# Kernel tuning notes

Hardware: AMD Instinct MI355X
Metric: run time of the kernel (lower is better)

Reference implementation:

```python
import jax, jax.numpy as jnp
import numpy as np

NUM_CLUSTERS = 16
HIDDEN = 1024
BOTTLENECK = 128
N_TOKENS = 65536


def setup_inputs() -> dict:
    key = jax.random.key(0)
    k_h, k_ids, k_w1, k_b1, k_w2, k_b2 = jax.random.split(key, 6)
    h = jax.random.normal(k_h, (N_TOKENS, HIDDEN), dtype=jnp.float32)
    cluster_ids = jax.random.randint(k_ids, (N_TOKENS,), 0, NUM_CLUSTERS)
    # Stacked per-cluster adapter params (torch Linear: y = x @ W.T + b; we store
    # already-transposed weights so forward is x @ W1[c]).
    s1 = 1.0 / np.sqrt(HIDDEN)
    s2 = 1.0 / np.sqrt(BOTTLENECK)
    W1 = jax.random.uniform(k_w1, (NUM_CLUSTERS, HIDDEN, BOTTLENECK), jnp.float32, -s1, s1)
    b1 = jax.random.uniform(k_b1, (NUM_CLUSTERS, BOTTLENECK), jnp.float32, -s1, s1)
    # Original inits these to zero; use small random values so grads are non-trivial.
    W2 = jax.random.uniform(k_w2, (NUM_CLUSTERS, BOTTLENECK, HIDDEN), jnp.float32, -s2, s2) * 0.02
    b2 = jax.random.uniform(k_b2, (NUM_CLUSTERS, HIDDEN), jnp.float32, -s2, s2) * 0.02
    return {"h": h, "cluster_ids": cluster_ids, "W1": W1, "b1": b1, "W2": W2, "b2": b2}


def reference(h, cluster_ids, W1, b1, W2, b2):
    # h: [N, H]; cluster_ids: [N]; W1: [K, H, B]; b1: [K, B]; W2: [K, B, H]; b2: [K, H]
    # out[n] = h[n] + adapter_{cluster_ids[n]}(h[n])
    K = W1.shape[0]
    out = jnp.zeros_like(h)
    for c in range(K):  # fixed small expert count; select per-token result via where
        mid = jax.nn.gelu(h @ W1[c] + b1[c], approximate=False)  # [N, B]
        y = h + mid @ W2[c] + b2[c]                               # [N, H]
        out = jnp.where((cluster_ids == c)[:, None], y, out)
    return out
```

## Files before the change

kernel.cpp:

```cpp
#include <hip/hip_runtime.h>
#include <hip/hip_bf16.h>
#include <math.h>

#define NUM_CLUSTERS 16
#define HIDDEN 1024
#define BOT 128
#define NTOK 65536

typedef __attribute__((ext_vector_type(8))) short bf16x8;
typedef __attribute__((ext_vector_type(4))) float f32x4;

typedef __attribute__((address_space(3))) unsigned int lds_u32;
typedef const __attribute__((address_space(1))) unsigned int glb_u32;

__device__ __forceinline__ void gload16(const void* g, void* l) {
  __builtin_amdgcn_global_load_lds((glb_u32*)g, (lds_u32*)l, 16, 0, 0);
}

__device__ __forceinline__ unsigned short f2bf(float x) {
  union { float f; unsigned u; } v; v.f = x;
  unsigned r = v.u + 0x7fffu + ((v.u >> 16) & 1u);
  return (unsigned short)(r >> 16);
}

__device__ __forceinline__ bf16x8 pack8(float4 a, float4 b) {
  bf16x8 r;
  r[0] = (short)f2bf(a.x); r[1] = (short)f2bf(a.y);
  r[2] = (short)f2bf(a.z); r[3] = (short)f2bf(a.w);
  r[4] = (short)f2bf(b.x); r[5] = (short)f2bf(b.y);
  r[6] = (short)f2bf(b.z); r[7] = (short)f2bf(b.w);
  return r;
}

#define SWZS(row, sidx) ((sidx) ^ (((row) & 7) << 3))
#define SW4(row, fidx) ((fidx) ^ (((row) & 7) << 2))

#define VMW(n) asm volatile("s_waitcnt vmcnt(" #n ")" ::: "memory")
#define SBAR()                                  \
  do {                                          \
    __builtin_amdgcn_sched_barrier(0);          \
    __builtin_amdgcn_s_barrier();               \
    __builtin_amdgcn_sched_barrier(0);          \
  } while (0)
#define LGKM0() asm volatile("s_waitcnt lgkmcnt(0)" ::: "memory")

__device__ __forceinline__ int xcd_swz(int bid, int nwg) {
  const int nx = 8;
  int q = nwg / nx, r = nwg % nx;
  int xcd = bid % nx, idx = bid / nx;
  int b = (xcd < r) ? xcd * (q + 1) : r * (q + 1) + (xcd - r) * q;
  return b + idx;
}


__global__ void k_zero(int* p) {
  if (threadIdx.x < 64) p[threadIdx.x] = 0;
}

__global__ void k_hist(const int* __restrict__ ids, int* __restrict__ counts) {
  __shared__ int lh[NUM_CLUSTERS];
  if (threadIdx.x < NUM_CLUSTERS) lh[threadIdx.x] = 0;
  __syncthreads();
  int i = blockIdx.x * blockDim.x + threadIdx.x;
  int stride = gridDim.x * blockDim.x;
  for (; i < NTOK; i += stride) atomicAdd(&lh[ids[i]], 1);
  __syncthreads();
  if (threadIdx.x < NUM_CLUSTERS) atomicAdd(&counts[threadIdx.x], lh[threadIdx.x]);
}

__global__ void k_scan(const int* __restrict__ counts, int* __restrict__ offsets,
                       int* __restrict__ cursor) {
  if (threadIdx.x == 0 && blockIdx.x == 0) {
    int s = 0;
    for (int c = 0; c < NUM_CLUSTERS; ++c) {
      offsets[c] = s; cursor[c] = s; s += counts[c];
    }
    offsets[NUM_CLUSTERS] = s;
  }
}

__global__ void k_scatter(const int* __restrict__ ids, int* cursor,
                          int* __restrict__ perm) {
  __shared__ int lh[NUM_CLUSTERS], lbase[NUM_CLUSTERS];
  const int tid = threadIdx.x;
  if (tid < NUM_CLUSTERS) lh[tid] = 0;
  __syncthreads();
  const int i = blockIdx.x * 256 + tid;
  const int cc = ids[i];
  const int r = atomicAdd(&lh[cc], 1);
  __syncthreads();
  if (tid < NUM_CLUSTERS) lbase[tid] = atomicAdd(&cursor[tid], lh[tid]);
  __syncthreads();
  perm[lbase[cc] + r] = i;
}

__global__ void k_w1til(const float* __restrict__ W1, unsigned short* __restrict__ outw) {
  const int id = blockIdx.x * 256 + threadIdx.x;
  const int c  = id >> 14;
  const int ks = (id >> 10) & 15;
  const int q  = id & 1023;
  const int o  = q << 4;
  const int row = o >> 7;
  const int lb  = (o & 127) ^ ((row & 7) << 4);
  const int k0  = ks * 64 + (lb >> 1);
  const float* src = W1 + ((size_t)c * HIDDEN + k0) * BOT + row;
  unsigned short v[8];
  #pragma unroll
  for (int j = 0; j < 8; ++j) v[j] = f2bf(src[(size_t)j * BOT]);
  *(uint4*)((char*)outw + ((size_t)(c * 16 + ks)) * 16384 + o) = *(const uint4*)v;
}

__global__ void k_w2til(const float* __restrict__ W2, unsigned short* __restrict__ outw) {
  const int id = blockIdx.x * 256 + threadIdx.x;
  const int c  = id >> 14;
  const int nc = (id >> 10) & 15;
  const int q  = id & 1023;
  const int o  = q << 4;
  const int row = o >> 8;
  const int lb  = (o & 255) ^ ((row & 7) << 4);
  const int b0  = lb >> 1;
  const int n   = nc * 64 + row;
  const float* src = W2 + ((size_t)c * BOT + b0) * HIDDEN + n;
  unsigned short v[8];
  #pragma unroll
  for (int j = 0; j < 8; ++j) v[j] = f2bf(src[(size_t)j * HIDDEN]);
  *(uint4*)((char*)outw + ((size_t)(c * 16 + nc)) * 16384 + o) = *(const uint4*)v;
}

__device__ __forceinline__ bool locate(const int* offsets, int bid, int TMv,
                                       int& c, int& base, int& nvalid) {
  int t = bid;
  for (c = 0; c < NUM_CLUSTERS; ++c) {
    int cnt = offsets[c + 1] - offsets[c];
    int nt = (cnt + TMv - 1) / TMv;
    if (t < nt) {
      base = offsets[c] + t * TMv;
      nvalid = min(TMv, offsets[c + 1] - base);
      return true;
    }
    t -= nt;
  }
  return false;
}


__global__ __launch_bounds__(512, 6) void k_gemm1(
    const float* __restrict__ h, const float* __restrict__ b1g,
    const unsigned short* __restrict__ W1til, const int* __restrict__ offsets,
    const int* __restrict__ perm, unsigned short* __restrict__ midg) {

  __shared__ __align__(16) unsigned short sA[2][4096];
  __shared__ __align__(16) unsigned short sB[2][8192];
  __shared__ int sTok[64];

  const int tid = threadIdx.x;
  const int l = tid & 63, w = tid >> 6;
  const int lr = l & 15, lg = l >> 4;
  const int wr = w >> 2, wc = w & 3;

  const int nwg = NTOK / 64 + NUM_CLUSTERS;
  int c, base, nvalid;
  if (!locate(offsets, xcd_swz(blockIdx.x, nwg), 64, c, base, nvalid)) return;

  if (tid < 64) sTok[tid] = perm[base + min(tid, nvalid - 1)];
  __syncthreads();

  const unsigned short* w1base = W1til + (size_t)c * 16 * 8192;
  const int row = tid >> 3, o8 = tid & 7;
  const float* hrow = h + (long)sTok[row] * HIDDEN + o8 * 8;

  float4 vaA[2], vaB[2];
  vaA[0] = *(const float4*)(hrow);       vaA[1] = *(const float4*)(hrow + 4);
  gload16(w1base + tid * 8, &sB[0][tid * 8]);
  gload16(w1base + 4096 + tid * 8, &sB[0][4096 + tid * 8]);
  vaB[0] = *(const float4*)(hrow + 64);  vaB[1] = *(const float4*)(hrow + 68);
  *(bf16x8*)&sA[0][SWZS(row, row * 64 + o8 * 8)] = pack8(vaA[0], vaA[1]);
  LGKM0();
  SBAR();

  f32x4 acc[2][2];
  #pragma unroll
  for (int i = 0; i < 2; ++i)
    #pragma unroll
    for (int j = 0; j < 2; ++j) { f32x4 z = {0.f, 0.f, 0.f, 0.f}; acc[i][j] = z; }

#define G1_MFMA(CUR)                                                          \
  do {                                                                        \
    _Pragma("unroll")                                                         \
    for (int kk = 0; kk < 2; ++kk) {                                          \
      bf16x8 af[2], bfr[2];                                                   \
      _Pragma("unroll")                                                       \
      for (int mf = 0; mf < 2; ++mf) {                                        \
        const int m = wr * 32 + mf * 16 + lr;                                 \
        af[mf] = *(const bf16x8*)&sA[CUR][SWZS(m, m * 64 + kk * 32 + lg * 8)];\
      }                                                                       \
      _Pragma("unroll")                                                       \
      for (int nf = 0; nf < 2; ++nf) {                                        \
        const int rn = wc * 32 + nf * 16 + lr;                                \
        bfr[nf] = *(const bf16x8*)&sB[CUR][SWZS(rn, rn * 64 + kk * 32 + lg * 8)]; \
      }                                                                       \
      _Pragma("unroll")                                                       \
      for (int mf = 0; mf < 2; ++mf)                                          \
        _Pragma("unroll")                                                     \
        for (int nf = 0; nf < 2; ++nf)                                        \
          acc[mf][nf] = __builtin_amdgcn_mfma_f32_16x16x32_bf16(              \
              af[mf], bfr[nf], acc[mf][nf], 0, 0, 0);                         \
    }                                                                         \
  } while (0)

#define G1_ISSUE_B(T, NXT)                                                    \
  do {                                                                        \
    const unsigned short* w1s = w1base + (T + 1) * 8192;                      \
    gload16(w1s + tid * 8, &sB[NXT][tid * 8]);                                \
    gload16(w1s + 4096 + tid * 8, &sB[NXT][4096 + tid * 8]);                  \
  } while (0)

#define G1_STAGE(SRC, NXT)                                                    \
  do {                                                                        \
    *(bf16x8*)&sA[NXT][SWZS(row, row * 64 + o8 * 8)] = pack8(SRC[0], SRC[1]); \
    LGKM0();                                                                  \
    SBAR();                                                                   \
  } while (0)

  for (int tp = 0; tp < 14; tp += 2) {
    G1_ISSUE_B(tp, 1);
    vaA[0] = *(const float4*)(hrow + (tp + 2) * 64);
    vaA[1] = *(const float4*)(hrow + (tp + 2) * 64 + 4);
    VMW(6);
    SBAR();
    G1_MFMA(0);
    G1_STAGE(vaB, 1);
    G1_ISSUE_B(tp + 1, 0);
    vaB[0] = *(const float4*)(hrow + (tp + 3) * 64);
    vaB[1] = *(const float4*)(hrow + (tp + 3) * 64 + 4);
    VMW(6);
    SBAR();
    G1_MFMA(1);
    G1_STAGE(vaA, 0);
  }
  G1_ISSUE_B(14, 1);
  VMW(4);
  SBAR();
  G1_MFMA(0);
  G1_STAGE(vaB, 1);
  VMW(0);
  SBAR();
  G1_MFMA(1);

  float b1v[2];
  #pragma unroll
  for (int nf = 0; nf < 2; ++nf) b1v[nf] = b1g[c * BOT + wc * 32 + nf * 16 + lr];
  #pragma unroll
  for (int mf = 0; mf < 2; ++mf) {
    #pragma unroll
    for (int nf = 0; nf < 2; ++nf) {
      #pragma unroll
      for (int r = 0; r < 4; ++r) {
        float x = acc[mf][nf][r] + b1v[nf];
        float g = 0.5f * x * (1.0f + erff(x * 0.70710678118654752f));
        const int m = wr * 32 + mf * 16 + lg * 4 + r;
        if (m < nvalid) {
          const int n = wc * 32 + nf * 16 + lr;
          midg[(size_t)(base + m) * BOT + n] = f2bf(g);
        }
      }
    }
  }
}


__global__ __launch_bounds__(512, 6) void k_gemm2(
    const float* __restrict__ h, const float* __restrict__ b2g,
    const unsigned short* __restrict__ W2til, const int* __restrict__ offsets,
    const int* __restrict__ perm, const unsigned short* __restrict__ midg,
    float* __restrict__ out) {

  __shared__ __align__(16) unsigned short sM[8192];
  __shared__ __align__(16) unsigned short sB[2][8192];
  __shared__ int sTok[64];

  const int tid = threadIdx.x;
  const int l = tid & 63, w = tid >> 6;
  const int lr = l & 15, lg = l >> 4;
  const int wr = w >> 2, wc = w & 3;

  const int nwg = NTOK / 64 + NUM_CLUSTERS;
  int c, base, nvalid;
  if (!locate(offsets, xcd_swz(blockIdx.x, nwg), 64, c, base, nvalid)) return;

  if (tid < 64) sTok[tid] = perm[base + min(tid, nvalid - 1)];

  const unsigned short* w2base = W2til + (size_t)c * 16 * 8192;

  {
    const int row = tid >> 3, oct = tid & 7;
    const int srow = base + min(row, nvalid - 1);
    const uint4* ms = (const uint4*)(midg + (size_t)srow * BOT + oct * 16);
    uint4 m0 = ms[0], m1 = ms[1];
    gload16(w2base + tid * 8, &sB[0][tid * 8]);
    gload16(w2base + 4096 + tid * 8, &sB[0][4096 + tid * 8]);
    *(uint4*)&sM[SWZS(row, row * 128 + oct * 16)]     = m0;
    *(uint4*)&sM[SWZS(row, row * 128 + oct * 16 + 8)] = m1;
  }
  LGKM0();
  SBAR();

  const int erow = tid >> 3, eo = tid & 7;
  const long etok = (long)sTok[erow] * HIDDEN;
  const float* hrow = h + etok;
  float* orow = out + etok;
  const bool evalid = erow < nvalid;

  for (int nc = 0; nc < 16; ++nc) {
    const int cur = nc & 1;
    float4 hv0 = *(const float4*)(hrow + nc * 64 + eo * 8);
    float4 hv1 = *(const float4*)(hrow + nc * 64 + eo * 8 + 4);
    float4 bv0 = *(const float4*)(b2g + c * HIDDEN + nc * 64 + eo * 8);
    float4 bv1 = *(const float4*)(b2g + c * HIDDEN + nc * 64 + eo * 8 + 4);
    if (nc < 15) {
      const unsigned short* w2s = w2base + (nc + 1) * 8192;
      gload16(w2s + tid * 8, &sB[cur ^ 1][tid * 8]);
      gload16(w2s + 4096 + tid * 8, &sB[cur ^ 1][4096 + tid * 8]);
    }
    if (nc == 0 || nc == 15) { VMW(6); } else { VMW(8); }
    SBAR();

    f32x4 acc[2];
    { f32x4 z = {0.f, 0.f, 0.f, 0.f}; acc[0] = z; acc[1] = z; }
    #pragma unroll
    for (int kk = 0; kk < 4; ++kk) {
      bf16x8 af[2], bf1;
      #pragma unroll
      for (int mf = 0; mf < 2; ++mf) {
        const int m = wr * 32 + mf * 16 + lr;
        af[mf] = *(const bf16x8*)&sM[SWZS(m, m * 128 + kk * 32 + lg * 8)];
      }
      const int rn = wc * 16 + lr;
      bf1 = *(const bf16x8*)&sB[cur][SWZS(rn, rn * 128 + kk * 32 + lg * 8)];
      #pragma unroll
      for (int mf = 0; mf < 2; ++mf)
        acc[mf] = __builtin_amdgcn_mfma_f32_16x16x32_bf16(af[mf], bf1, acc[mf], 0, 0, 0);
    }
    SBAR();

    float* sOutF = (float*)&sB[cur][0];
    #pragma unroll
    for (int mf = 0; mf < 2; ++mf) {
      #pragma unroll
      for (int r = 0; r < 4; ++r) {
        const int m = wr * 32 + mf * 16 + lg * 4 + r;
        const int n = wc * 16 + lr;
        sOutF[SW4(m, m * 64 + n)] = acc[mf][r];
      }
    }
    LGKM0();
    SBAR();

    if (evalid) {
      const int fb = erow * 64 + eo * 8;
      const float4 y0 = *(const float4*)&sOutF[SW4(erow, fb)];
      const float4 y1 = *(const float4*)&sOutF[SW4(erow, fb + 4)];
      float4 o0, o1;
      o0.x = y0.x + hv0.x + bv0.x; o0.y = y0.y + hv0.y + bv0.y;
      o0.z = y0.z + hv0.z + bv0.z; o0.w = y0.w + hv0.w + bv0.w;
      o1.x = y1.x + hv1.x + bv1.x; o1.y = y1.y + hv1.y + bv1.y;
      o1.z = y1.z + hv1.z + bv1.z; o1.w = y1.w + hv1.w + bv1.w;
      *(float4*)(orow + nc * 64 + eo * 8)     = o0;
      *(float4*)(orow + nc * 64 + eo * 8 + 4) = o1;
    }
    SBAR();
  }
}

#define FSWZ(row, sidx) ((sidx) ^ (((row) & 7) << 3))

__global__ __launch_bounds__(256, 2) void k_fused(
    const float* __restrict__ h, const float* __restrict__ b1g,
    const float* __restrict__ b2g, const unsigned short* __restrict__ W1til,
    const unsigned short* __restrict__ W2til, const int* __restrict__ offsets,
    const int* __restrict__ perm, float* __restrict__ out) {

  __shared__ __align__(16) unsigned short sAB[16384];
  __shared__ __align__(16) unsigned short sMid[16384];
  __shared__ int sTok[128];

  const int tid = threadIdx.x;
  const int l = tid & 63, w = tid >> 6;
  const int wr = w >> 1, wc = w & 1;
  const int lr = l & 15, lg = l >> 4;

  int c, base, nvalid;
  if (!locate(offsets, blockIdx.x, 128, c, base, nvalid)) return;

  if (tid < 128) sTok[tid] = perm[base + min(tid, nvalid - 1)];
  __syncthreads();

  const unsigned short* w1base = W1til + (size_t)c * 16 * 8192;
  const unsigned short* w2base = W2til + (size_t)c * 16 * 8192;

  const int arow = tid >> 1, ahalf = tid & 1;
  const long htok = (long)sTok[arow] * HIDDEN;

  f32x4 acc[4][4];
  #pragma unroll
  for (int i = 0; i < 4; ++i)
    #pragma unroll
    for (int j = 0; j < 4; ++j) { f32x4 z = {0.f, 0.f, 0.f, 0.f}; acc[i][j] = z; }

  for (int ks = 0; ks < 16; ++ks) {
    __syncthreads();
    const unsigned short* w1s = w1base + ks * 8192;
    #pragma unroll
    for (int j = 0; j < 4; ++j)
      gload16(w1s + j * 2048 + tid * 8, &sAB[8192 + j * 2048 + tid * 8]);
    {
      const float* hp = h + htok + ks * 64 + ahalf * 32;
      float4 v0 = *(const float4*)(hp + 0),  v1 = *(const float4*)(hp + 4);
      float4 v2 = *(const float4*)(hp + 8),  v3 = *(const float4*)(hp + 12);
      float4 v4 = *(const float4*)(hp + 16), v5 = *(const float4*)(hp + 20);
      float4 v6 = *(const float4*)(hp + 24), v7 = *(const float4*)(hp + 28);
      const int sb = arow * 64 + ahalf * 32;
      *(bf16x8*)&sAB[FSWZ(arow, sb + 0)]  = pack8(v0, v1);
      *(bf16x8*)&sAB[FSWZ(arow, sb + 8)]  = pack8(v2, v3);
      *(bf16x8*)&sAB[FSWZ(arow, sb + 16)] = pack8(v4, v5);
      *(bf16x8*)&sAB[FSWZ(arow, sb + 24)] = pack8(v6, v7);
    }
    __syncthreads();
    #pragma unroll
    for (int kk = 0; kk < 2; ++kk) {
      bf16x8 af[4], bfr[4];
      #pragma unroll
      for (int mf = 0; mf < 4; ++mf) {
        const int row = wr * 64 + mf * 16 + lr;
        af[mf] = *(const bf16x8*)&sAB[FSWZ(row, row * 64 + kk * 32 + lg * 8)];
      }
      #pragma unroll
      for (int nf = 0; nf < 4; ++nf) {
        const int rn = wc * 64 + nf * 16 + lr;
        bfr[nf] = *(const bf16x8*)&sAB[8192 + FSWZ(rn, rn * 64 + kk * 32 + lg * 8)];
      }
      #pragma unroll
      for (int mf = 0; mf < 4; ++mf)
        #pragma unroll
        for (int nf = 0; nf < 4; ++nf)
          acc[mf][nf] = __builtin_amdgcn_mfma_f32_16x16x32_bf16(af[mf], bfr[nf], acc[mf][nf], 0, 0, 0);
    }
  }

  float b1v[4];
  #pragma unroll
  for (int nf = 0; nf < 4; ++nf) b1v[nf] = b1g[c * BOT + wc * 64 + nf * 16 + lr];
  #pragma unroll
  for (int mf = 0; mf < 4; ++mf)
    #pragma unroll
    for (int nf = 0; nf < 4; ++nf)
      #pragma unroll
      for (int r = 0; r < 4; ++r) {
        float x = acc[mf][nf][r] + b1v[nf];
        float g = 0.5f * x * (1.0f + erff(x * 0.70710678118654752f));
        const int m = wr * 64 + mf * 16 + lg * 4 + r;
        const int n = wc * 64 + nf * 16 + lr;
        sMid[FSWZ(m, m * 128 + n)] = f2bf(g);
      }

  for (int nc = 0; nc < 16; ++nc) {
    __syncthreads();
    #pragma unroll
    for (int j = 0; j < 4; ++j)
      gload16(w2base + nc * 8192 + j * 2048 + tid * 8, &sAB[j * 2048 + tid * 8]);
    __syncthreads();

    f32x4 a2[4][2];
    #pragma unroll
    for (int i = 0; i < 4; ++i)
      #pragma unroll
      for (int j = 0; j < 2; ++j) { f32x4 z = {0.f, 0.f, 0.f, 0.f}; a2[i][j] = z; }

    #pragma unroll
    for (int kk = 0; kk < 4; ++kk) {
      bf16x8 af[4], bfr[2];
      #pragma unroll
      for (int mf = 0; mf < 4; ++mf) {
        const int m = wr * 64 + mf * 16 + lr;
        af[mf] = *(const bf16x8*)&sMid[FSWZ(m, m * 128 + kk * 32 + lg * 8)];
      }
      #pragma unroll
      for (int nf = 0; nf < 2; ++nf) {
        const int rn = wc * 32 + nf * 16 + lr;
        bfr[nf] = *(const bf16x8*)&sAB[FSWZ(rn, rn * 128 + kk * 32 + lg * 8)];
      }
      #pragma unroll
      for (int mf = 0; mf < 4; ++mf)
        #pragma unroll
        for (int nf = 0; nf < 2; ++nf)
          a2[mf][nf] = __builtin_amdgcn_mfma_f32_16x16x32_bf16(af[mf], bfr[nf], a2[mf][nf], 0, 0, 0);
    }

    #pragma unroll
    for (int nf = 0; nf < 2; ++nf) {
      const int nn = nc * 64 + wc * 32 + nf * 16 + lr;
      const float b2v = b2g[c * HIDDEN + nn];
      #pragma unroll
      for (int mf = 0; mf < 4; ++mf)
        #pragma unroll
        for (int r = 0; r < 4; ++r) {
          const int m = wr * 64 + mf * 16 + lg * 4 + r;
          if (m < nvalid) {
            const long tk = (long)sTok[m] * HIDDEN;
            out[tk + nn] = h[tk + nn] + a2[mf][nf][r] + b2v;
          }
        }
    }
  }
}

extern "C" void kernel_launch(void* const* d_in, const int* in_sizes, int n_in,
                              void* d_out, int out_size, void* d_ws, size_t ws_size,
                              hipStream_t stream) {
  const float* h   = (const float*)d_in[0];
  const int*   ids = (const int*)d_in[1];
  const float* W1  = (const float*)d_in[2];
  const float* b1  = (const float*)d_in[3];
  const float* W2  = (const float*)d_in[4];
  const float* b2  = (const float*)d_in[5];
  float* out = (float*)d_out;

  char* ws = (char*)d_ws;
  int* counts  = (int*)ws;
  int* cursor  = (int*)(ws + 64);
  int* offsets = (int*)(ws + 128);
  int* perm    = (int*)(ws + 256);
  unsigned short* W1til = (unsigned short*)(ws + 262400);
  unsigned short* W2til = W1til + (size_t)16 * 16 * 8192;
  unsigned short* midg  = W2til + (size_t)16 * 16 * 8192;
  const size_t need = 262400 + 2 * (size_t)16 * 16 * 8192 * 2 +
                      (size_t)NTOK * BOT * 2;

  k_zero<<<1, 64, 0, stream>>>(counts);
  k_hist<<<256, 256, 0, stream>>>(ids, counts);
  k_scan<<<1, 64, 0, stream>>>(counts, offsets, cursor);
  k_scatter<<<NTOK / 256, 256, 0, stream>>>(ids, cursor, perm);
  k_w1til<<<1024, 256, 0, stream>>>(W1, W1til);
  k_w2til<<<1024, 256, 0, stream>>>(W2, W2til);

  if (ws_size >= need) {
    const int nwg = NTOK / 64 + NUM_CLUSTERS;
    k_gemm1<<<nwg, 512, 0, stream>>>(h, b1, W1til, offsets, perm, midg);
    k_gemm2<<<nwg, 512, 0, stream>>>(h, b2, W2til, offsets, perm, midg, out);
  } else {
    k_fused<<<NTOK / 128 + NUM_CLUSTERS, 256, 0, stream>>>(
        h, b1, b2, W1til, W2til, offsets, perm, out);
  }
}
```

Measured before the change: 269.9 us.

## Process two token tiles per workgroup in gemm kernels and tighten wait scheduling

Both grouped GEMM kernels now launch half as many workgroups, and each one loops over two consecutive 64-token tiles. The per-tile prologue is repeated inside the loop. The vmcnt waits are wrapped in sched_barriers and the loads are pinned in place, with waits changed to depend on the pipeline stage. The aim is to cut workgroup launch and tail overhead and to get more predictable overlap of loads with MFMA. The cost is less parallelism, and the second tile's prologue is serialized after the first tile's epilogue.

```diff
diff --git a/kernel.cpp b/kernel.cpp
--- a/kernel.cpp
+++ b/kernel.cpp
@@ -6,6 +6,7 @@
 #define HIDDEN 1024
 #define BOT 128
 #define NTOK 65536
+#define NPAIRS ((NTOK / 64 + NUM_CLUSTERS) / 2)
 
 typedef __attribute__((ext_vector_type(8))) short bf16x8;
 typedef __attribute__((ext_vector_type(4))) float f32x4;
@@ -35,12 +36,18 @@
 #define SWZS(row, sidx) ((sidx) ^ (((row) & 7) << 3))
 #define SW4(row, fidx) ((fidx) ^ (((row) & 7) << 2))
 
-#define VMW(n) asm volatile("s_waitcnt vmcnt(" #n ")" ::: "memory")
+#define SCB() __builtin_amdgcn_sched_barrier(0)
+#define VMW(n)                                          \
+  do {                                                  \
+    SCB();                                              \
+    asm volatile("s_waitcnt vmcnt(" #n ")" ::: "memory"); \
+    SCB();                                              \
+  } while (0)
 #define SBAR()                                  \
   do {                                          \
-    __builtin_amdgcn_sched_barrier(0);          \
+    SCB();                                      \
     __builtin_amdgcn_s_barrier();               \
-    __builtin_amdgcn_sched_barrier(0);          \
+    SCB();                                      \
   } while (0)
 #define LGKM0() asm volatile("s_waitcnt lgkmcnt(0)" ::: "memory")
 
@@ -157,32 +164,9 @@
   const int l = tid & 63, w = tid >> 6;
   const int lr = l & 15, lg = l >> 4;
   const int wr = w >> 2, wc = w & 3;
-
-  const int nwg = NTOK / 64 + NUM_CLUSTERS;
-  int c, base, nvalid;
-  if (!locate(offsets, xcd_swz(blockIdx.x, nwg), 64, c, base, nvalid)) return;
-
-  if (tid < 64) sTok[tid] = perm[base + min(tid, nvalid - 1)];
-  __syncthreads();
-
-  const unsigned short* w1base = W1til + (size_t)c * 16 * 8192;
   const int row = tid >> 3, o8 = tid & 7;
-  const float* hrow = h + (long)sTok[row] * HIDDEN + o8 * 8;
-
-  float4 vaA[2], vaB[2];
-  vaA[0] = *(const float4*)(hrow);       vaA[1] = *(const float4*)(hrow + 4);
-  gload16(w1base + tid * 8, &sB[0][tid * 8]);
-  gload16(w1base + 4096 + tid * 8, &sB[0][4096 + tid * 8]);
-  vaB[0] = *(const float4*)(hrow + 64);  vaB[1] = *(const float4*)(hrow + 68);
-  *(bf16x8*)&sA[0][SWZS(row, row * 64 + o8 * 8)] = pack8(vaA[0], vaA[1]);
-  LGKM0();
-  SBAR();
-
-  f32x4 acc[2][2];
-  #pragma unroll
-  for (int i = 0; i < 2; ++i)
-    #pragma unroll
-    for (int j = 0; j < 2; ++j) { f32x4 z = {0.f, 0.f, 0.f, 0.f}; acc[i][j] = z; }
+
+  const int pair = xcd_swz(blockIdx.x, NPAIRS);
 
 #define G1_MFMA(CUR)                                                          \
   do {                                                                        \
@@ -208,64 +192,87 @@
     }                                                                         \
   } while (0)
 
-#define G1_ISSUE_B(T, NXT)                                                    \
-  do {                                                                        \
-    const unsigned short* w1s = w1base + (T + 1) * 8192;                      \
-    gload16(w1s + tid * 8, &sB[NXT][tid * 8]);                                \
-    gload16(w1s + 4096 + tid * 8, &sB[NXT][4096 + tid * 8]);                  \
-  } while (0)
-
-#define G1_STAGE(SRC, NXT)                                                    \
-  do {                                                                        \
-    *(bf16x8*)&sA[NXT][SWZS(row, row * 64 + o8 * 8)] = pack8(SRC[0], SRC[1]); \
-    LGKM0();                                                                  \
-    SBAR();                                                                   \
-  } while (0)
-
-  for (int tp = 0; tp < 14; tp += 2) {
-    G1_ISSUE_B(tp, 1);
-    vaA[0] = *(const float4*)(hrow + (tp + 2) * 64);
-    vaA[1] = *(const float4*)(hrow + (tp + 2) * 64 + 4);
-    VMW(6);
+  for (int tt = 0; tt < 2; ++tt) {
+    int c, base, nvalid;
+    if (!locate(offsets, pair * 2 + tt, 64, c, base, nvalid)) break;
+
+    if (tid < 64) sTok[tid] = perm[base + min(tid, nvalid - 1)];
+    LGKM0();
     SBAR();
-    G1_MFMA(0);
-    G1_STAGE(vaB, 1);
-    G1_ISSUE_B(tp + 1, 0);
-    vaB[0] = *(const float4*)(hrow + (tp + 3) * 64);
-    vaB[1] = *(const float4*)(hrow + (tp + 3) * 64 + 4);
-    VMW(6);
+
+    const unsigned short* w1base = W1til + (size_t)c * 16 * 8192;
+    const float* hrow = h + (long)sTok[row] * HIDDEN + o8 * 8;
+
+    float4 vaA[2], vaB[2];
+    vaA[0] = *(const float4*)(hrow);       vaA[1] = *(const float4*)(hrow + 4);
+    SCB();
+    gload16(w1base + tid * 8, &sB[0][tid * 8]);
+    gload16(w1base + 4096 + tid * 8, &sB[0][4096 + tid * 8]);
+    SCB();
+    vaB[0] = *(const float4*)(hrow + 64);  vaB[1] = *(const float4*)(hrow + 68);
+    SCB();
+    *(bf16x8*)&sA[0][SWZS(row, row * 64 + o8 * 8)] = pack8(vaA[0], vaA[1]);
+    LGKM0();
+    VMW(2);
     SBAR();
-    G1_MFMA(1);
-    G1_STAGE(vaA, 0);
-  }
-  G1_ISSUE_B(14, 1);
-  VMW(4);
-  SBAR();
-  G1_MFMA(0);
-  G1_STAGE(vaB, 1);
-  VMW(0);
-  SBAR();
-  G1_MFMA(1);
-
-  float b1v[2];
-  #pragma unroll
-  for (int nf = 0; nf < 2; ++nf) b1v[nf] = b1g[c * BOT + wc * 32 + nf * 16 + lr];
-  #pragma unroll
-  for (int mf = 0; mf < 2; ++mf) {
-    #pragma unroll
-    for (int nf = 0; nf < 2; ++nf) {
-      #pragma unroll
-      for (int r = 0; r < 4; ++r) {
-        float x = acc[mf][nf][r] + b1v[nf];
-        float g = 0.5f * x * (1.0f + erff(x * 0.70710678118654752f));
-        const int m = wr * 32 + mf * 16 + lg * 4 + r;
-        if (m < nvalid) {
-          const int n = wc * 32 + nf * 16 + lr;
-          midg[(size_t)(base + m) * BOT + n] = f2bf(g);
+
+    f32x4 acc[2][2];
+    #pragma unroll
+    for (int i = 0; i < 2; ++i)
+      #pragma unroll
+      for (int j = 0; j < 2; ++j) { f32x4 z = {0.f, 0.f, 0.f, 0.f}; acc[i][j] = z; }
+
+    #pragma unroll
+    for (int t = 0; t < 16; ++t) {
+      const int cur = t & 1;
+      if (t < 15) {
+        const unsigned short* w1s = w1base + (t + 1) * 8192;
+        gload16(w1s + tid * 8, &sB[cur ^ 1][tid * 8]);
+        gload16(w1s + 4096 + tid * 8, &sB[cur ^ 1][4096 + tid * 8]);
+        SCB();
+      }
+      if (t < 14) {
+        if (t & 1) {
+          vaB[0] = *(const float4*)(hrow + (t + 2) * 64);
+          vaB[1] = *(const float4*)(hrow + (t + 2) * 64 + 4);
+        } else {
+          vaA[0] = *(const float4*)(hrow + (t + 2) * 64);
+          vaA[1] = *(const float4*)(hrow + (t + 2) * 64 + 4);
         }
-      }
-    }
-  }
+        SCB();
+      }
+      G1_MFMA(cur);
+      if (t < 15) {
+        const float4* src = ((t + 1) & 1) ? vaB : vaA;
+        *(bf16x8*)&sA[cur ^ 1][SWZS(row, row * 64 + o8 * 8)] = pack8(src[0], src[1]);
+        if (t < 14) { VMW(2); } else { VMW(0); }
+        LGKM0();
+        SBAR();
+      }
+    }
+
+    float b1v[2];
+    #pragma unroll
+    for (int nf = 0; nf < 2; ++nf) b1v[nf] = b1g[c * BOT + wc * 32 + nf * 16 + lr];
+    #pragma unroll
+    for (int mf = 0; mf < 2; ++mf) {
+      #pragma unroll
+      for (int nf = 0; nf < 2; ++nf) {
+        #pragma unroll
+        for (int r = 0; r < 4; ++r) {
+          float x = acc[mf][nf][r] + b1v[nf];
+          float g = 0.5f * x * (1.0f + erff(x * 0.70710678118654752f));
+          const int m = wr * 32 + mf * 16 + lg * 4 + r;
+          if (m < nvalid) {
+            const int n = wc * 32 + nf * 16 + lr;
+            midg[(size_t)(base + m) * BOT + n] = f2bf(g);
+          }
+        }
+      }
+    }
+    VMW(0);
+  }
+#undef G1_MFMA
 }
 
 
@@ -283,92 +290,100 @@
   const int l = tid & 63, w = tid >> 6;
   const int lr = l & 15, lg = l >> 4;
   const int wr = w >> 2, wc = w & 3;
-
-  const int nwg = NTOK / 64 + NUM_CLUSTERS;
-  int c, base, nvalid;
-  if (!locate(offsets, xcd_swz(blockIdx.x, nwg), 64, c, base, nvalid)) return;
-
-  if (tid < 64) sTok[tid] = perm[base + min(tid, nvalid - 1)];
-
-  const unsigned short* w2base = W2til + (size_t)c * 16 * 8192;
-
-  {
-    const int row = tid >> 3, oct = tid & 7;
-    const int srow = base + min(row, nvalid - 1);
-    const uint4* ms = (const uint4*)(midg + (size_t)srow * BOT + oct * 16);
-    uint4 m0 = ms[0], m1 = ms[1];
-    gload16(w2base + tid * 8, &sB[0][tid * 8]);
-    gload16(w2base + 4096 + tid * 8, &sB[0][4096 + tid * 8]);
-    *(uint4*)&sM[SWZS(row, row * 128 + oct * 16)]     = m0;
-    *(uint4*)&sM[SWZS(row, row * 128 + oct * 16 + 8)] = m1;
-  }
-  LGKM0();
-  SBAR();
-
   const int erow = tid >> 3, eo = tid & 7;
-  const long etok = (long)sTok[erow] * HIDDEN;
-  const float* hrow = h + etok;
-  float* orow = out + etok;
-  const bool evalid = erow < nvalid;
-
-  for (int nc = 0; nc < 16; ++nc) {
-    const int cur = nc & 1;
-    float4 hv0 = *(const float4*)(hrow + nc * 64 + eo * 8);
-    float4 hv1 = *(const float4*)(hrow + nc * 64 + eo * 8 + 4);
-    float4 bv0 = *(const float4*)(b2g + c * HIDDEN + nc * 64 + eo * 8);
-    float4 bv1 = *(const float4*)(b2g + c * HIDDEN + nc * 64 + eo * 8 + 4);
-    if (nc < 15) {
-      const unsigned short* w2s = w2base + (nc + 1) * 8192;
-      gload16(w2s + tid * 8, &sB[cur ^ 1][tid * 8]);
-      gload16(w2s + 4096 + tid * 8, &sB[cur ^ 1][4096 + tid * 8]);
-    }
-    if (nc == 0 || nc == 15) { VMW(6); } else { VMW(8); }
+
+  const int pair = xcd_swz(blockIdx.x, NPAIRS);
+
+  for (int tt = 0; tt < 2; ++tt) {
+    int c, base, nvalid;
+    if (!locate(offsets, pair * 2 + tt, 64, c, base, nvalid)) break;
+
+    if (tid < 64) sTok[tid] = perm[base + min(tid, nvalid - 1)];
+
+    const unsigned short* w2base = W2til + (size_t)c * 16 * 8192;
+
+    {
+      const int srow = base + min(erow, nvalid - 1);
+      const uint4* ms = (const uint4*)(midg + (size_t)srow * BOT + eo * 16);
+      uint4 m0 = ms[0], m1 = ms[1];
+      SCB();
+      gload16(w2base + tid * 8, &sB[0][tid * 8]);
+      gload16(w2base + 4096 + tid * 8, &sB[0][4096 + tid * 8]);
+      SCB();
+      *(uint4*)&sM[SWZS(erow, erow * 128 + eo * 16)]     = m0;
+      *(uint4*)&sM[SWZS(erow, erow * 128 + eo * 16 + 8)] = m1;
+    }
+    LGKM0();
+    VMW(0);
     SBAR();
 
-    f32x4 acc[2];
-    { f32x4 z = {0.f, 0.f, 0.f, 0.f}; acc[0] = z; acc[1] = z; }
-    #pragma unroll
-    for (int kk = 0; kk < 4; ++kk) {
-      bf16x8 af[2], bf1;
+    const long etok = (long)sTok[erow] * HIDDEN;
+    const float* hrow = h + etok;
+    float* orow = out + etok;
+    const bool evalid = erow < nvalid;
+
+    for (int nc = 0; nc < 16; ++nc) {
+      const int cur = nc & 1;
+      float4 hv0 = *(const float4*)(hrow + nc * 64 + eo * 8);
+      float4 hv1 = *(const float4*)(hrow + nc * 64 + eo * 8 + 4);
+      float4 bv0 = *(const float4*)(b2g + c * HIDDEN + nc * 64 + eo * 8);
+      float4 bv1 = *(const float4*)(b2g + c * HIDDEN + nc * 64 + eo * 8 + 4);
+      SCB();
+      if (nc < 15) {
+        const unsigned short* w2s = w2base + (nc + 1) * 8192;
+        gload16(w2s + tid * 8, &sB[cur ^ 1][tid * 8]);
+        gload16(w2s + 4096 + tid * 8, &sB[cur ^ 1][4096 + tid * 8]);
+        SCB();
+      }
+
+      f32x4 acc[2];
+      { f32x4 z = {0.f, 0.f, 0.f, 0.f}; acc[0] = z; acc[1] = z; }
+      #pragma unroll
+      for (int kk = 0; kk < 4; ++kk) {
+        bf16x8 af[2], bf1;
+        #pragma unroll
+        for (int mf = 0; mf < 2; ++mf) {
+          const int m = wr * 32 + mf * 16 + lr;
+          af[mf] = *(const bf16x8*)&sM[SWZS(m, m * 128 + kk * 32 + lg * 8)];
+        }
+        const int rn = wc * 16 + lr;
+        bf1 = *(const bf16x8*)&sB[cur][SWZS(rn, rn * 128 + kk * 32 + lg * 8)];
+        #pragma unroll
+        for (int mf = 0; mf < 2; ++mf)
+          acc[mf] = __builtin_amdgcn_mfma_f32_16x16x32_bf16(af[mf], bf1, acc[mf], 0, 0, 0);
+      }
+      SBAR();
+
+      float* sOutF = (float*)&sB[cur][0];
       #pragma unroll
       for (int mf = 0; mf < 2; ++mf) {
-        const int m = wr * 32 + mf * 16 + lr;
-        af[mf] = *(const bf16x8*)&sM[SWZS(m, m * 128 + kk * 32 + lg * 8)];
-      }
-      const int rn = wc * 16 + lr;
-      bf1 = *(const bf16x8*)&sB[cur][SWZS(rn, rn * 128 + kk * 32 + lg * 8)];
-      #pragma unroll
-      for (int mf = 0; mf < 2; ++mf)
-        acc[mf] = __builtin_amdgcn_mfma_f32_16x16x32_bf16(af[mf], bf1, acc[mf], 0, 0, 0);
-    }
-    SBAR();
-
-    float* sOutF = (float*)&sB[cur][0];
-    #pragma unroll
-    for (int mf = 0; mf < 2; ++mf) {
-      #pragma unroll
-      for (int r = 0; r < 4; ++r) {
-        const int m = wr * 32 + mf * 16 + lg * 4 + r;
-        const int n = wc * 16 + lr;
-        sOutF[SW4(m, m * 64 + n)] = acc[mf][r];
-      }
-    }
-    LGKM0();
-    SBAR();
-
-    if (evalid) {
-      const int fb = erow * 64 + eo * 8;
-      const float4 y0 = *(const float4*)&sOutF[SW4(erow, fb)];
-      const float4 y1 = *(const float4*)&sOutF[SW4(erow, fb + 4)];
-      float4 o0, o1;
-      o0.x = y0.x + hv0.x + bv0.x; o0.y = y0.y + hv0.y + bv0.y;
-      o0.z = y0.z + hv0.z + bv0.z; o0.w = y0.w + hv0.w + bv0.w;
-      o1.x = y1.x + hv1.x + bv1.x; o1.y = y1.y + hv1.y + bv1.y;
-      o1.z = y1.z + hv1.z + bv1.z; o1.w = y1.w + hv1.w + bv1.w;
-      *(float4*)(orow + nc * 64 + eo * 8)     = o0;
-      *(float4*)(orow + nc * 64 + eo * 8 + 4) = o1;
-    }
-    SBAR();
+        #pragma unroll
+        for (int r = 0; r < 4; ++r) {
+          const int m = wr * 32 + mf * 16 + lg * 4 + r;
+          const int n = wc * 16 + lr;
+          sOutF[SW4(m, m * 64 + n)] = acc[mf][r];
+        }
+      }
+      LGKM0();
+      SBAR();
+
+      if (evalid) {
+        const int fb = erow * 64 + eo * 8;
+        const float4 y0 = *(const float4*)&sOutF[SW4(erow, fb)];
+        const float4 y1 = *(const float4*)&sOutF[SW4(erow, fb + 4)];
+        float4 o0, o1;
+        o0.x = y0.x + hv0.x + bv0.x; o0.y = y0.y + hv0.y + bv0.y;
+        o0.z = y0.z + hv0.z + bv0.z; o0.w = y0.w + hv0.w + bv0.w;
+        o1.x = y1.x + hv1.x + bv1.x; o1.y = y1.y + hv1.y + bv1.y;
+        o1.z = y1.z + hv1.z + bv1.z; o1.w = y1.w + hv1.w + bv1.w;
+        *(float4*)(orow + nc * 64 + eo * 8)     = o0;
+        *(float4*)(orow + nc * 64 + eo * 8 + 4) = o1;
+      }
+      if (nc < 15) {
+        VMW(2);
+        SBAR();
+      }
+    }
   }
 }
 
@@ -431,8 +446,8 @@
       bf16x8 af[4], bfr[4];
       #pragma unroll
       for (int mf = 0; mf < 4; ++mf) {
-        const int row = wr * 64 + mf * 16 + lr;
-        af[mf] = *(const bf16x8*)&sAB[FSWZ(row, row * 64 + kk * 32 + lg * 8)];
+        const int rw = wr * 64 + mf * 16 + lr;
+        af[mf] = *(const bf16x8*)&sAB[FSWZ(rw, rw * 64 + kk * 32 + lg * 8)];
       }
       #pragma unroll
       for (int nf = 0; nf < 4; ++nf) {
@@ -544,9 +559,8 @@
   k_w2til<<<1024, 256, 0, stream>>>(W2, W2til);
 
   if (ws_size >= need) {
-    const int nwg = NTOK / 64 + NUM_CLUSTERS;
-    k_gemm1<<<nwg, 512, 0, stream>>>(h, b1, W1til, offsets, perm, midg);
-    k_gemm2<<<nwg, 512, 0, stream>>>(h, b2, W2til, offsets, perm, midg, out);
+    k_gemm1<<<NPAIRS, 512, 0, stream>>>(h, b1, W1til, offsets, perm, midg);
+    k_gemm2<<<NPAIRS, 512, 0, stream>>>(h, b2, W2til, offsets, perm, midg, out);
   } else {
     k_fused<<<NTOK / 128 + NUM_CLUSTERS, 256, 0, stream>>>(
         h, b1, b2, W1til, W2til, offsets, perm, out);
```

Measured after the change: 313.5 us. 1.16x slower.
